# Kernel tuning notes

Measured on AMD Instinct MI355X. Metric: run time of the kernel, lower is better.

## Reference

```python
import jax, jax.numpy as jnp
import numpy as np

B, N, F, H = 2, 2048, 1024, 16
HD = F // H
SQRT_D = float(np.sqrt(F))  # note: module scales by sqrt(in_c), not sqrt(head_dim)


def setup_inputs() -> dict:
    key = jax.random.key(0)
    ks = jax.random.split(key, 9)
    s = 1.0 / np.sqrt(F)
    mk = lambda k: jax.random.uniform(k, (F, F), jnp.float32, -s, s)
    mb = lambda k: jax.random.uniform(k, (F,), jnp.float32, -s, s)
    return {
        "x": jax.random.normal(ks[0], (B, N, F), jnp.float32),
        "Wq": mk(ks[1]), "bq": mb(ks[2]),
        "Wk": mk(ks[3]), "bk": mb(ks[4]),
        "Wv": mk(ks[5]), "bv": mb(ks[6]),
        "Wo": mk(ks[7]), "bo": mb(ks[8]),
    }


def reference(x, Wq, bq, Wk, bk, Wv, bv, Wo, bo):
    b, n, f = x.shape
    # projections (torch Linear: x @ W.T + b); view to (b, n, h, hd)
    q = (x @ Wq.T + bq).reshape(b, n, H, HD)
    k = (x @ Wk.T + bk).reshape(b, n, H, HD)
    v = (x @ Wv.T + bv).reshape(b, n, H, HD)
    score = jnp.einsum('bihd,bjhd->bhij', q, k)
    attn = jax.nn.softmax(score / SQRT_D, axis=-1)
    o = jnp.einsum('bhij,bjhd->bihd', attn, v).reshape(b, n, f)
    return o @ Wo.T + bo
```

## Files before the change

kernel.cpp:

```cpp
#include <hip/hip_runtime.h>
#include <hip/hip_bf16.h>
#include <stdint.h>
#include <stddef.h>

typedef __bf16 bf16;
typedef __attribute__((ext_vector_type(8))) __bf16 bf16x8;
typedef __attribute__((ext_vector_type(4))) __bf16 bf16x4;
typedef __attribute__((ext_vector_type(2))) __bf16 bf16x2;
typedef __attribute__((ext_vector_type(4))) float f32x4;

#define MFMA16(a, b, c) __builtin_amdgcn_mfma_f32_16x16x32_bf16(a, b, c, 0, 0, 0)

#define BB 2
#define SEQ 2048
#define FDIM 1024
#define NH 16
#define HD 64
#define M_TOK 4096
#define N_QKV 3072

#define CSC 0.04508422f

__device__ __forceinline__ void gll16(const bf16* g, bf16* l) {
    __builtin_amdgcn_global_load_lds(
        (const __attribute__((address_space(1))) void*)g,
        (__attribute__((address_space(3))) void*)l, 16, 0, 0);
}

__device__ __forceinline__ bf16 pack_bf16(float f) {
    uint32_t u = __builtin_bit_cast(uint32_t, f);
    uint16_t h = (uint16_t)((u + 0x8000u) >> 16);
    return __builtin_bit_cast(bf16, h);
}

__device__ __forceinline__ uint32_t pk2(float a, float b) {
#if __has_builtin(__builtin_amdgcn_cvt_pk_bf16_f32)
    bf16x2 t = __builtin_amdgcn_cvt_pk_bf16_f32(a, b);
    return __builtin_bit_cast(uint32_t, t);
#else
    uint32_t ua = __builtin_bit_cast(uint32_t, a) + 0x8000u;
    uint32_t ub = __builtin_bit_cast(uint32_t, b) + 0x8000u;
    return __builtin_amdgcn_perm(ub, ua, 0x07060302);
#endif
}

__global__ __launch_bounds__(256) void convert_k(
    const float* __restrict__ x,
    const float* __restrict__ Wq, const float* __restrict__ bq,
    const float* __restrict__ Wk, const float* __restrict__ bk,
    const float* __restrict__ Wv, const float* __restrict__ bv,
    const float* __restrict__ Wo,
    bf16* __restrict__ xb, bf16* __restrict__ Wcat, bf16* __restrict__ Wob,
    float* __restrict__ bcat)
{
    const int tid = blockIdx.x * blockDim.x + threadIdx.x;
    const int nt = gridDim.x * blockDim.x;
    const int NX4 = M_TOK * FDIM / 4;
    const int NW4 = FDIM * FDIM / 4;

    for (int i = tid; i < NX4; i += nt) {
        float4 v = ((const float4*)x)[i];
        bf16x4 o; o[0] = (bf16)v.x; o[1] = (bf16)v.y; o[2] = (bf16)v.z; o[3] = (bf16)v.w;
        ((bf16x4*)xb)[i] = o;
    }
    for (int i = tid; i < NW4; i += nt) {
        float4 v = ((const float4*)Wq)[i];
        bf16x4 o;
        o[0] = (bf16)(v.x * CSC); o[1] = (bf16)(v.y * CSC);
        o[2] = (bf16)(v.z * CSC); o[3] = (bf16)(v.w * CSC);
        ((bf16x4*)Wcat)[i] = o;
        v = ((const float4*)Wk)[i];
        o[0] = (bf16)v.x; o[1] = (bf16)v.y; o[2] = (bf16)v.z; o[3] = (bf16)v.w;
        ((bf16x4*)Wcat)[NW4 + i] = o;
        v = ((const float4*)Wv)[i];
        o[0] = (bf16)v.x; o[1] = (bf16)v.y; o[2] = (bf16)v.z; o[3] = (bf16)v.w;
        ((bf16x4*)Wcat)[2 * NW4 + i] = o;
        v = ((const float4*)Wo)[i];
        o[0] = (bf16)v.x; o[1] = (bf16)v.y; o[2] = (bf16)v.z; o[3] = (bf16)v.w;
        ((bf16x4*)Wob)[i] = o;
    }
    for (int i = tid; i < FDIM; i += nt) {
        bcat[i] = bq[i] * CSC;
        bcat[FDIM + i] = bk[i];
        bcat[2 * FDIM + i] = bv[i];
    }
}

template<int MT>
__global__ __launch_bounds__(256) void gemm_bt(
    const bf16* __restrict__ A,
    const bf16* __restrict__ Bw,
    const float* __restrict__ bias,
    bf16* __restrict__ Cb,
    float* __restrict__ Cf,
    bf16* __restrict__ VtOut,
    int M, int N, int K)
{
    constexpr int RI = MT / 32;
    __shared__ __align__(16) bf16 As[2][MT * 32];
    __shared__ __align__(16) bf16 Bs[2][128 * 32];

    const int tid = threadIdx.x;
    const int lane = tid & 63;
    const int wave = tid >> 6;
    const int m0 = blockIdx.y * MT;
    const int n0 = blockIdx.x * 128;
    const int wm = (wave >> 1) * (MT / 2);
    const int wn = (wave & 1) * 64;
    const int lrow = lane & 15;
    const int lk8 = (lane >> 4) * 8;

    f32x4 acc[RI][4] = {};

    const int srow = wave * 16 + (lane >> 2);
    const int scol = (lane & 3) * 8;
    const bf16* Ag = A + (size_t)(m0 + srow) * K + scol;
    const bf16* Bg = Bw + (size_t)(n0 + srow) * K + scol;
    const int wo = (wave * 16) * 32;

    gll16(Ag, &As[0][wo]);
    if (MT == 128) gll16(Ag + (size_t)64 * K, &As[0][wo + 2048]);
    gll16(Bg, &Bs[0][wo]);
    gll16(Bg + (size_t)64 * K, &Bs[0][wo + 2048]);

    for (int k0 = 0, it = 0; k0 < K; k0 += 32, ++it) {
        const int cur = it & 1;
        __syncthreads();

        if (k0 + 32 < K) {
            const int nxt = cur ^ 1;
            gll16(Ag + k0 + 32, &As[nxt][wo]);
            if (MT == 128) gll16(Ag + (size_t)64 * K + k0 + 32, &As[nxt][wo + 2048]);
            gll16(Bg + k0 + 32, &Bs[nxt][wo]);
            gll16(Bg + (size_t)64 * K + k0 + 32, &Bs[nxt][wo + 2048]);
        }

        bf16x8 af[RI], bfr[4];
#pragma unroll
        for (int s = 0; s < RI; ++s)
            af[s] = *(const bf16x8*)&As[cur][(wm + s * 16 + lrow) * 32 + lk8];
#pragma unroll
        for (int s = 0; s < 4; ++s)
            bfr[s] = *(const bf16x8*)&Bs[cur][(wn + s * 16 + lrow) * 32 + lk8];
#pragma unroll
        for (int i = 0; i < RI; ++i)
#pragma unroll
            for (int j = 0; j < 4; ++j)
                acc[i][j] = MFMA16(af[i], bfr[j], acc[i][j]);
    }

    const int r0 = (lane >> 4) * 4;
    if (MT == 128 && VtOut && n0 >= 2048) {
        const int bql = (m0 >> 11);
#pragma unroll
        for (int i = 0; i < RI; ++i) {
#pragma unroll
            for (int j = 0; j < 4; ++j) {
                const int col = n0 + wn + j * 16 + lrow;
                const float bsv = bias[col];
                const int vh = col - 2048;
                const int row = m0 + wm + i * 16 + r0;
                const int jj = row & (SEQ - 1);
                const int g = jj & 63;
                const int jj2 = (jj & ~63) | ((g >> 5) << 5)
                              | (((g >> 2) & 3) << 3) | (((g >> 4) & 1) << 2);
                bf16x4 vv;
#pragma unroll
                for (int r = 0; r < 4; ++r)
                    vv[r] = pack_bf16(acc[i][j][r] + bsv);
                *(bf16x4*)&VtOut[((size_t)bql * 16 * 64 + vh) * SEQ + jj2] = vv;
            }
        }
        return;
    }
#pragma unroll
    for (int i = 0; i < RI; ++i) {
#pragma unroll
        for (int j = 0; j < 4; ++j) {
            const int col = n0 + wn + j * 16 + lrow;
            const float bsv = bias[col];
#pragma unroll
            for (int r = 0; r < 4; ++r) {
                const int row = m0 + wm + i * 16 + r0 + r;
                const float v = acc[i][j][r] + bsv;
                if (Cb) Cb[(size_t)row * N + col] = pack_bf16(v);
                else    Cf[(size_t)row * N + col] = v;
            }
        }
    }
}

__global__ __launch_bounds__(128) void attn_k(
    const bf16* __restrict__ QKV,
    const bf16* __restrict__ Vt,
    bf16* __restrict__ O)
{
    const int bx = blockIdx.x;
    const int bh = (bx & 7) + 8 * ((bx >> 3) & 3);
    const int qblk = bx >> 5;
    const int b = bh >> 4;
    const int h = bh & 15;
    const int lane = threadIdx.x & 63;
    const int wave = threadIdx.x >> 6;
    const int lrow = lane & 15;
    const int quad = lane >> 4;
    const int lk8 = quad * 8;

    __shared__ __align__(16) bf16 Ks[2][2][128 * 32];
    __shared__ __align__(16) bf16 Vs[2][4][64 * 32];

    const size_t base = (size_t)b * SEQ * N_QKV;
    const bf16* Qp = QKV + base + h * HD;
    const bf16* Kp = QKV + base + FDIM + h * HD;
    const bf16* Vtp = Vt + (size_t)bh * HD * SEQ;

    const int qr0 = qblk * 128 + wave * 64;

    bf16x8 qf[4][2];
#pragma unroll
    for (int qt = 0; qt < 4; ++qt)
#pragma unroll
        for (int ks = 0; ks < 2; ++ks)
            qf[qt][ks] = *(const bf16x8*)(Qp + (size_t)(qr0 + qt * 16 + lrow) * N_QKV
                                          + ks * 32 + lk8);

    bf16x8 ones8;
#pragma unroll
    for (int e = 0; e < 8; ++e) ones8[e] = (bf16)1.0f;

    const f32x4 zf = {0.f, 0.f, 0.f, 0.f};

    f32x4 o[4][4] = {};
    f32x4 o4[4] = {};

    const int sr = lane >> 2;
    const int sc = (lane & 3) * 8;
    const bf16* kg = Kp + (size_t)sr * N_QKV + sc;
    const bf16* vg = Vtp + (size_t)sr * SEQ + sc;

    if (wave == 0) {
#pragma unroll
        for (int i = 0; i < 8; ++i) {
            gll16(kg + (size_t)i * 16 * N_QKV, &Ks[0][0][i * 16 * 32]);
            gll16(kg + (size_t)i * 16 * N_QKV + 32, &Ks[0][1][i * 16 * 32]);
        }
    } else {
#pragma unroll
        for (int p = 0; p < 4; ++p)
#pragma unroll
            for (int i = 0; i < 4; ++i)
                gll16(vg + (size_t)i * 16 * SEQ + p * 32, &Vs[0][p][i * 16 * 32]);
    }
    kg += (size_t)128 * N_QKV;
    vg += 128;

    for (int jt = 0; jt < SEQ / 128; ++jt) {
        const int cur = jt & 1;
        __syncthreads();

        if (jt + 1 < SEQ / 128) {
            const int nxt = cur ^ 1;
            if (wave == 0) {
#pragma unroll
                for (int i = 0; i < 8; ++i) {
                    gll16(kg + (size_t)i * 16 * N_QKV, &Ks[nxt][0][i * 16 * 32]);
                    gll16(kg + (size_t)i * 16 * N_QKV + 32, &Ks[nxt][1][i * 16 * 32]);
                }
            } else {
#pragma unroll
                for (int p = 0; p < 4; ++p)
#pragma unroll
                    for (int i = 0; i < 4; ++i)
                        gll16(vg + (size_t)i * 16 * SEQ + p * 32, &Vs[nxt][p][i * 16 * 32]);
            }
            kg += (size_t)128 * N_QKV;
            vg += 128;
        }

#pragma unroll
        for (int p = 0; p < 4; ++p) {
            f32x4 Sp[2][4];
#pragma unroll
            for (int m = 0; m < 2; ++m) {
                const int jn = 2 * p + m;
                bf16x8 kb0 = *(const bf16x8*)&Ks[cur][0][(jn * 16 + lrow) * 32 + lk8];
                bf16x8 kb1 = *(const bf16x8*)&Ks[cur][1][(jn * 16 + lrow) * 32 + lk8];
#pragma unroll
                for (int qt = 0; qt < 4; ++qt) {
                    Sp[m][qt] = MFMA16(kb0, qf[qt][0], zf);
                    Sp[m][qt] = MFMA16(kb1, qf[qt][1], Sp[m][qt]);
                }
            }

            union { bf16x8 v; uint32_t d[4]; } pb[4];
#pragma unroll
            for (int qt = 0; qt < 4; ++qt) {
                const f32x4 s0 = Sp[0][qt];
                const f32x4 s1 = Sp[1][qt];
                pb[qt].d[0] = pk2(__builtin_amdgcn_exp2f(s0[0]),
                                  __builtin_amdgcn_exp2f(s0[1]));
                pb[qt].d[1] = pk2(__builtin_amdgcn_exp2f(s0[2]),
                                  __builtin_amdgcn_exp2f(s0[3]));
                pb[qt].d[2] = pk2(__builtin_amdgcn_exp2f(s1[0]),
                                  __builtin_amdgcn_exp2f(s1[1]));
                pb[qt].d[3] = pk2(__builtin_amdgcn_exp2f(s1[2]),
                                  __builtin_amdgcn_exp2f(s1[3]));
                o4[qt] = MFMA16(ones8, pb[qt].v, o4[qt]);
            }

#pragma unroll
            for (int df = 0; df < 4; ++df) {
                bf16x8 vA = *(const bf16x8*)&Vs[cur][p][(df * 16 + lrow) * 32 + lk8];
#pragma unroll
                for (int qt = 0; qt < 4; ++qt)
                    o[qt][df] = MFMA16(vA, pb[qt].v, o[qt][df]);
            }
        }
    }

#pragma unroll
    for (int qt = 0; qt < 4; ++qt) {
        const float inv = 1.0f / o4[qt][0];
        const int q = qr0 + qt * 16 + lrow;
#pragma unroll
        for (int df = 0; df < 4; ++df) {
            bf16x4 vv;
#pragma unroll
            for (int r = 0; r < 4; ++r)
                vv[r] = pack_bf16(o[qt][df][r] * inv);
            *(bf16x4*)&O[(size_t)(b * SEQ + q) * FDIM + h * HD + df * 16 + quad * 4] = vv;
        }
    }
}

extern "C" void kernel_launch(void* const* d_in, const int* in_sizes, int n_in,
                              void* d_out, int out_size, void* d_ws, size_t ws_size,
                              hipStream_t stream) {
    (void)in_sizes; (void)n_in; (void)out_size; (void)ws_size;
    const float* x  = (const float*)d_in[0];
    const float* Wq = (const float*)d_in[1];
    const float* bq = (const float*)d_in[2];
    const float* Wk = (const float*)d_in[3];
    const float* bk = (const float*)d_in[4];
    const float* Wv = (const float*)d_in[5];
    const float* bv = (const float*)d_in[6];
    const float* Wo = (const float*)d_in[7];
    const float* bo = (const float*)d_in[8];
    float* out = (float*)d_out;

    char* ws = (char*)d_ws;
    bf16* xb    = (bf16*)(ws);
    bf16* Wcat  = (bf16*)(ws + 8388608);
    bf16* Wob   = (bf16*)(ws + 14680064);
    float* bcat = (float*)(ws + 16777216);
    bf16* QKV   = (bf16*)(ws + 16789504);
    bf16* Vt    = (bf16*)(ws + 41955328);
    bf16* Ob    = xb;

    convert_k<<<dim3(1024), dim3(256), 0, stream>>>(x, Wq, bq, Wk, bk, Wv, bv, Wo,
                                                    xb, Wcat, Wob, bcat);
    gemm_bt<128><<<dim3(N_QKV / 128, M_TOK / 128), dim3(256), 0, stream>>>(
        xb, Wcat, bcat, QKV, nullptr, Vt, M_TOK, N_QKV, FDIM);
    attn_k<<<dim3((SEQ / 128) * BB * NH), dim3(128), 0, stream>>>(QKV, Vt, Ob);
    gemm_bt<64><<<dim3(FDIM / 128, M_TOK / 64), dim3(256), 0, stream>>>(
        Ob, Wob, bo, nullptr, out, nullptr, M_TOK, FDIM, FDIM);
}
```

Measured before the change: 192.7 us.

## Split attention KV range in two and combine halves with float atomics

```diff
diff --git a/kernel.cpp b/kernel.cpp
--- a/kernel.cpp
+++ b/kernel.cpp
@@ -49,9 +49,7 @@
     const float* __restrict__ Wq, const float* __restrict__ bq,
     const float* __restrict__ Wk, const float* __restrict__ bk,
     const float* __restrict__ Wv, const float* __restrict__ bv,
-    const float* __restrict__ Wo,
-    bf16* __restrict__ xb, bf16* __restrict__ Wcat, bf16* __restrict__ Wob,
-    float* __restrict__ bcat)
+    bf16* __restrict__ xb, bf16* __restrict__ Wcat, float* __restrict__ bcat)
 {
     const int tid = blockIdx.x * blockDim.x + threadIdx.x;
     const int nt = gridDim.x * blockDim.x;
@@ -75,15 +73,20 @@
         v = ((const float4*)Wv)[i];
         o[0] = (bf16)v.x; o[1] = (bf16)v.y; o[2] = (bf16)v.z; o[3] = (bf16)v.w;
         ((bf16x4*)Wcat)[2 * NW4 + i] = o;
-        v = ((const float4*)Wo)[i];
-        o[0] = (bf16)v.x; o[1] = (bf16)v.y; o[2] = (bf16)v.z; o[3] = (bf16)v.w;
-        ((bf16x4*)Wob)[i] = o;
     }
     for (int i = tid; i < FDIM; i += nt) {
         bcat[i] = bq[i] * CSC;
         bcat[FDIM + i] = bk[i];
         bcat[2 * FDIM + i] = bv[i];
     }
+}
+
+__global__ __launch_bounds__(256) void zero_k(float4* __restrict__ p, int n4)
+{
+    const int tid = blockIdx.x * blockDim.x + threadIdx.x;
+    const int nt = gridDim.x * blockDim.x;
+    const float4 z = {0.f, 0.f, 0.f, 0.f};
+    for (int i = tid; i < n4; i += nt) p[i] = z;
 }
 
 template<int MT>
@@ -94,7 +97,7 @@
     bf16* __restrict__ Cb,
     float* __restrict__ Cf,
     bf16* __restrict__ VtOut,
-    int M, int N, int K)
+    int M, int N, int K, int lda)
 {
     constexpr int RI = MT / 32;
     __shared__ __align__(16) bf16 As[2][MT * 32];
@@ -114,12 +117,12 @@
 
     const int srow = wave * 16 + (lane >> 2);
     const int scol = (lane & 3) * 8;
-    const bf16* Ag = A + (size_t)(m0 + srow) * K + scol;
+    const bf16* Ag = A + (size_t)(m0 + srow) * lda + scol;
     const bf16* Bg = Bw + (size_t)(n0 + srow) * K + scol;
     const int wo = (wave * 16) * 32;
 
     gll16(Ag, &As[0][wo]);
-    if (MT == 128) gll16(Ag + (size_t)64 * K, &As[0][wo + 2048]);
+    if (MT == 128) gll16(Ag + (size_t)64 * lda, &As[0][wo + 2048]);
     gll16(Bg, &Bs[0][wo]);
     gll16(Bg + (size_t)64 * K, &Bs[0][wo + 2048]);
 
@@ -130,7 +133,7 @@
         if (k0 + 32 < K) {
             const int nxt = cur ^ 1;
             gll16(Ag + k0 + 32, &As[nxt][wo]);
-            if (MT == 128) gll16(Ag + (size_t)64 * K + k0 + 32, &As[nxt][wo + 2048]);
+            if (MT == 128) gll16(Ag + (size_t)64 * lda + k0 + 32, &As[nxt][wo + 2048]);
             gll16(Bg + k0 + 32, &Bs[nxt][wo]);
             gll16(Bg + (size_t)64 * K + k0 + 32, &Bs[nxt][wo + 2048]);
         }
@@ -193,11 +196,14 @@
 __global__ __launch_bounds__(128) void attn_k(
     const bf16* __restrict__ QKV,
     const bf16* __restrict__ Vt,
-    bf16* __restrict__ O)
+    float* __restrict__ Oacc,
+    float* __restrict__ L)
 {
     const int bx = blockIdx.x;
     const int bh = (bx & 7) + 8 * ((bx >> 3) & 3);
-    const int qblk = bx >> 5;
+    const int rest = bx >> 5;
+    const int qblk = rest & 15;
+    const int jhalf = rest >> 4;
     const int b = bh >> 4;
     const int h = bh & 15;
     const int lane = threadIdx.x & 63;
@@ -206,8 +212,8 @@
     const int quad = lane >> 4;
     const int lk8 = quad * 8;
 
-    __shared__ __align__(16) bf16 Ks[2][2][128 * 32];
-    __shared__ __align__(16) bf16 Vs[2][4][64 * 32];
+    __shared__ __align__(16) bf16 Ks[2][2][64 * 32];
+    __shared__ __align__(16) bf16 Vs[2][2][64 * 32];
 
     const size_t base = (size_t)b * SEQ * N_QKV;
     const bf16* Qp = QKV + base + h * HD;
@@ -215,6 +221,7 @@
     const bf16* Vtp = Vt + (size_t)bh * HD * SEQ;
 
     const int qr0 = qblk * 128 + wave * 64;
+    const int jbase = jhalf * (SEQ / 2);
 
     bf16x8 qf[4][2];
 #pragma unroll
@@ -235,50 +242,51 @@
 
     const int sr = lane >> 2;
     const int sc = (lane & 3) * 8;
-    const bf16* kg = Kp + (size_t)sr * N_QKV + sc;
-    const bf16* vg = Vtp + (size_t)sr * SEQ + sc;
+    const bf16* kg = Kp + (size_t)(jbase + sr) * N_QKV + sc;
+    const bf16* vg = Vtp + (size_t)sr * SEQ + jbase + sc;
 
     if (wave == 0) {
 #pragma unroll
-        for (int i = 0; i < 8; ++i) {
+        for (int i = 0; i < 4; ++i) {
             gll16(kg + (size_t)i * 16 * N_QKV, &Ks[0][0][i * 16 * 32]);
             gll16(kg + (size_t)i * 16 * N_QKV + 32, &Ks[0][1][i * 16 * 32]);
         }
     } else {
 #pragma unroll
-        for (int p = 0; p < 4; ++p)
-#pragma unroll
-            for (int i = 0; i < 4; ++i)
-                gll16(vg + (size_t)i * 16 * SEQ + p * 32, &Vs[0][p][i * 16 * 32]);
-    }
-    kg += (size_t)128 * N_QKV;
-    vg += 128;
-
-    for (int jt = 0; jt < SEQ / 128; ++jt) {
+        for (int i = 0; i < 4; ++i) {
+            gll16(vg + (size_t)i * 16 * SEQ, &Vs[0][0][i * 16 * 32]);
+            gll16(vg + (size_t)i * 16 * SEQ + 32, &Vs[0][1][i * 16 * 32]);
+        }
+    }
+    kg += (size_t)64 * N_QKV;
+    vg += 64;
+
+    const int NJT = (SEQ / 2) / 64;
+    for (int jt = 0; jt < NJT; ++jt) {
         const int cur = jt & 1;
         __syncthreads();
 
-        if (jt + 1 < SEQ / 128) {
+        if (jt + 1 < NJT) {
             const int nxt = cur ^ 1;
             if (wave == 0) {
 #pragma unroll
-                for (int i = 0; i < 8; ++i) {
+                for (int i = 0; i < 4; ++i) {
                     gll16(kg + (size_t)i * 16 * N_QKV, &Ks[nxt][0][i * 16 * 32]);
                     gll16(kg + (size_t)i * 16 * N_QKV + 32, &Ks[nxt][1][i * 16 * 32]);
                 }
             } else {
 #pragma unroll
-                for (int p = 0; p < 4; ++p)
-#pragma unroll
-                    for (int i = 0; i < 4; ++i)
-                        gll16(vg + (size_t)i * 16 * SEQ + p * 32, &Vs[nxt][p][i * 16 * 32]);
-            }
-            kg += (size_t)128 * N_QKV;
-            vg += 128;
-        }
-
-#pragma unroll
-        for (int p = 0; p < 4; ++p) {
+                for (int i = 0; i < 4; ++i) {
+                    gll16(vg + (size_t)i * 16 * SEQ, &Vs[nxt][0][i * 16 * 32]);
+                    gll16(vg + (size_t)i * 16 * SEQ + 32, &Vs[nxt][1][i * 16 * 32]);
+                }
+            }
+            kg += (size_t)64 * N_QKV;
+            vg += 64;
+        }
+
+#pragma unroll
+        for (int p = 0; p < 2; ++p) {
             f32x4 Sp[2][4];
 #pragma unroll
             for (int m = 0; m < 2; ++m) {
@@ -320,16 +328,47 @@
 
 #pragma unroll
     for (int qt = 0; qt < 4; ++qt) {
-        const float inv = 1.0f / o4[qt][0];
         const int q = qr0 + qt * 16 + lrow;
-#pragma unroll
-        for (int df = 0; df < 4; ++df) {
-            bf16x4 vv;
+        if (quad == 0)
+            unsafeAtomicAdd(&L[bh * SEQ + q], o4[qt][0]);
+        float* od = &Oacc[(size_t)(b * SEQ + q) * FDIM + h * HD + quad * 4];
+#pragma unroll
+        for (int df = 0; df < 4; ++df)
 #pragma unroll
             for (int r = 0; r < 4; ++r)
-                vv[r] = pack_bf16(o[qt][df][r] * inv);
-            *(bf16x4*)&O[(size_t)(b * SEQ + q) * FDIM + h * HD + df * 16 + quad * 4] = vv;
-        }
+                unsafeAtomicAdd(od + df * 16 + r, o[qt][df][r]);
+    }
+}
+
+__global__ __launch_bounds__(256) void norm_k(
+    const float* __restrict__ Oacc, const float* __restrict__ L,
+    const float* __restrict__ Wo,
+    bf16* __restrict__ QKV, bf16* __restrict__ WobOut)
+{
+    const int tid = blockIdx.x * blockDim.x + threadIdx.x;
+    const int nt = gridDim.x * blockDim.x;
+    const int NO4 = M_TOK * FDIM / 4;
+    const int NW4 = FDIM * FDIM / 4;
+
+    for (int i = tid; i < NO4; i += nt) {
+        const int token = i >> 8;
+        const int c4 = i & 255;
+        const int bq = token;
+        const int h = c4 >> 4;
+        const int b = token >> 11;
+        const int q = token & (SEQ - 1);
+        const float inv = 1.0f / L[(b * NH + h) * SEQ + q];
+        float4 v = ((const float4*)Oacc)[i];
+        bf16x4 o;
+        o[0] = pack_bf16(v.x * inv); o[1] = pack_bf16(v.y * inv);
+        o[2] = pack_bf16(v.z * inv); o[3] = pack_bf16(v.w * inv);
+        *(bf16x4*)&QKV[(size_t)bq * N_QKV + 2 * FDIM + c4 * 4] = o;
+    }
+    for (int i = tid; i < NW4; i += nt) {
+        float4 v = ((const float4*)Wo)[i];
+        bf16x4 o;
+        o[0] = (bf16)v.x; o[1] = (bf16)v.y; o[2] = (bf16)v.z; o[3] = (bf16)v.w;
+        ((bf16x4*)WobOut)[i] = o;
     }
 }
 
@@ -349,19 +388,33 @@
     float* out = (float*)d_out;
 
     char* ws = (char*)d_ws;
-    bf16* xb    = (bf16*)(ws);
-    bf16* Wcat  = (bf16*)(ws + 8388608);
-    bf16* Wob   = (bf16*)(ws + 14680064);
-    float* bcat = (float*)(ws + 16777216);
-    bf16* QKV   = (bf16*)(ws + 16789504);
-    bf16* Vt    = (bf16*)(ws + 41955328);
-    bf16* Ob    = xb;
-
-    convert_k<<<dim3(1024), dim3(256), 0, stream>>>(x, Wq, bq, Wk, bk, Wv, bv, Wo,
-                                                    xb, Wcat, Wob, bcat);
+    bf16*  xb    = (bf16*)(ws);
+    bf16*  Wcat  = (bf16*)(ws + 8388608);
+    float* Oacc  = (float*)(ws);
+    float* L     = (float*)(ws + 16777216 - 262144 + 262144);
+    float* bcat  = (float*)(ws + 16777216);
+    bf16*  QKV   = (bf16*)(ws + 16789504);
+    bf16*  Vt    = (bf16*)(ws + 41955328);
+    bf16*  Wob   = Vt;
+    L = (float*)(ws + 16777216 - 524288);
+    L = (float*)(ws + 16515072);
+    L = (float*)(ws + 41955328 + 2097152);
+
+    convert_k<<<dim3(1024), dim3(256), 0, stream>>>(x, Wq, bq, Wk, bk, Wv, bv,
+                                                    xb, Wcat, bcat);
     gemm_bt<128><<<dim3(N_QKV / 128, M_TOK / 128), dim3(256), 0, stream>>>(
-        xb, Wcat, bcat, QKV, nullptr, Vt, M_TOK, N_QKV, FDIM);
-    attn_k<<<dim3((SEQ / 128) * BB * NH), dim3(128), 0, stream>>>(QKV, Vt, Ob);
+        xb, Wcat, bcat, QKV, nullptr, Vt, M_TOK, N_QKV, FDIM, FDIM);
+    {
+        float* Lfix = (float*)(ws + 14680064 + 0);
+        (void)Lfix;
+    }
+    L = (float*)(ws + 14680064);
+    L = (float*)(ws + 50343936);
+
+    zero_k<<<dim3(512), dim3(256), 0, stream>>>((float4*)Oacc, (16777216) / 16);
+    zero_k<<<dim3(64), dim3(256), 0, stream>>>((float4*)L, 262144 / 16);
+    attn_k<<<dim3((SEQ / 128) * BB * NH * 2), dim3(128), 0, stream>>>(QKV, Vt, Oacc, L);
+    norm_k<<<dim3(1024), dim3(256), 0, stream>>>(Oacc, L, Wo, QKV, Wob);
     gemm_bt<64><<<dim3(FDIM / 128, M_TOK / 64), dim3(256), 0, stream>>>(
-        Ob, Wob, bo, nullptr, out, nullptr, M_TOK, FDIM, FDIM);
-}
+        QKV + 2 * FDIM, Wob, bo, nullptr, out, nullptr, M_TOK, FDIM, FDIM, N_QKV);
+}
```

Measured after the change: 293.2 us. 1.52x slower.
